# Optimization experiments

Measured on AMD Instinct MI355X. Metric: run time of the kernel, lower is better.

Reference implementation:

```python
import jax, jax.numpy as jnp
import numpy as np

N = 4096
BATCH = 8192


def setup_inputs() -> dict:
    key = jax.random.key(0)
    x = jax.random.normal(key, (BATCH, N), dtype=jnp.float32)
    return {"x": x}


def reference(x):
    # Radix-2 butterfly network (Fast Walsh-Hadamard Transform):
    # at stage s, positions i and i ^ (2**s) are combined as (a+b, a-b).
    B, n = x.shape
    num_stages = int(np.log2(n))
    r = x
    for stage in range(num_stages):  # fixed small loop over log2(n) stages
        stride = 2 ** stage
        # pairs (i, i+stride) live in blocks of 2*stride
        r4 = r.reshape(B, n // (2 * stride), 2, stride)
        a = r4[:, :, 0, :]
        b = r4[:, :, 1, :]
        r = jnp.stack([a + b, a - b], axis=2).reshape(B, n)
    return r
```

## Files before the change

kernel.cpp:

```cpp
#include <hip/hip_runtime.h>


#define N 4096
#define LDS_STRIDE 17

__device__ __forceinline__ void h16(float r[16]) {
    #pragma unroll
    for (int s = 1; s < 16; s <<= 1) {
        #pragma unroll
        for (int m = 0; m < 16; ++m) {
            if (!(m & s)) {
                float x = r[m], y = r[m ^ s];
                r[m]     = x + y;
                r[m ^ s] = x - y;
            }
        }
    }
}

__global__ __launch_bounds__(256) void fwht4096_kernel(const float* __restrict__ in,
                                                       float* __restrict__ out) {
    __shared__ float lds[256 * LDS_STRIDE];

    const int t = threadIdx.x;
    const long long row = blockIdx.x;
    const float* __restrict__ rowIn  = in  + row * (long long)N;
    float* __restrict__       rowOut = out + row * (long long)N;

    float r[16];

    #pragma unroll
    for (int q = 0; q < 4; ++q) {
        const float4 v = *reinterpret_cast<const float4*>(rowIn + t * 16 + q * 4);
        r[q * 4 + 0] = v.x; r[q * 4 + 1] = v.y;
        r[q * 4 + 2] = v.z; r[q * 4 + 3] = v.w;
    }

    h16(r);

    #pragma unroll
    for (int i = 0; i < 16; ++i) lds[LDS_STRIDE * t + i] = r[i];
    __syncthreads();

    const int a = t & 15;
    const int c = t >> 4;
    #pragma unroll
    for (int k = 0; k < 16; ++k)
        r[k] = lds[LDS_STRIDE * (c * 16 + k) + a];

    h16(r);

    __syncthreads();
    #pragma unroll
    for (int k = 0; k < 16; ++k)
        lds[LDS_STRIDE * (c * 16 + k) + a] = r[k];
    __syncthreads();

    const int b = t >> 4;
    #pragma unroll
    for (int k = 0; k < 16; ++k)
        r[k] = lds[LDS_STRIDE * (k * 16 + b) + a];

    h16(r);

    __syncthreads();
    #pragma unroll
    for (int k = 0; k < 16; ++k)
        lds[LDS_STRIDE * (k * 16 + b) + a] = r[k];
    __syncthreads();

    #pragma unroll
    for (int i = 0; i < 16; ++i)
        r[i] = lds[LDS_STRIDE * t + i];

    #pragma unroll
    for (int q = 0; q < 4; ++q) {
        float4 v;
        v.x = r[q * 4 + 0]; v.y = r[q * 4 + 1];
        v.z = r[q * 4 + 2]; v.w = r[q * 4 + 3];
        *reinterpret_cast<float4*>(rowOut + t * 16 + q * 4) = v;
    }
}

extern "C" void kernel_launch(void* const* d_in, const int* in_sizes, int n_in,
                              void* d_out, int out_size, void* d_ws, size_t ws_size,
                              hipStream_t stream) {
    const float* x = (const float*)d_in[0];
    float* y = (float*)d_out;
    const int rows = in_sizes[0] / N;
    fwht4096_kernel<<<rows, 256, 0, stream>>>(x, y);
}
```

Measured before the change: 234.8 us.

## Swizzle LDS layout, drop padding, write final stage directly to global

Replaces the padded LDS (stride 17) with an unpadded 4096-float buffer that uses an XOR swizzle, so the first write can use float4 stores without bank conflicts. The second stage reads and writes back in place with no barrier in between, and the third stage writes straight to global memory with coalesced per-thread strided stores. This removes one LDS round trip and two barriers and reduces LDS usage, and it raises the launch-bounds occupancy hint. The trade-off is scalar global stores in place of float4 stores, plus swizzle index arithmetic.

```diff
diff --git a/kernel.cpp b/kernel.cpp
--- a/kernel.cpp
+++ b/kernel.cpp
@@ -2,7 +2,6 @@
 
 
 #define N 4096
-#define LDS_STRIDE 17
 
 __device__ __forceinline__ void h16(float r[16]) {
     #pragma unroll
@@ -18,9 +17,9 @@
     }
 }
 
-__global__ __launch_bounds__(256) void fwht4096_kernel(const float* __restrict__ in,
-                                                       float* __restrict__ out) {
-    __shared__ float lds[256 * LDS_STRIDE];
+__global__ __launch_bounds__(256, 8) void fwht4096_kernel(const float* __restrict__ in,
+                                                          float* __restrict__ out) {
+    __shared__ float lds[N];
 
     const int t = threadIdx.x;
     const long long row = blockIdx.x;
@@ -30,55 +29,50 @@
     float r[16];
 
     #pragma unroll
-    for (int q = 0; q < 4; ++q) {
-        const float4 v = *reinterpret_cast<const float4*>(rowIn + t * 16 + q * 4);
-        r[q * 4 + 0] = v.x; r[q * 4 + 1] = v.y;
-        r[q * 4 + 2] = v.z; r[q * 4 + 3] = v.w;
+    for (int j = 0; j < 4; ++j) {
+        const float4 v = *reinterpret_cast<const float4*>(rowIn + t * 16 + j * 4);
+        r[j * 4 + 0] = v.x; r[j * 4 + 1] = v.y;
+        r[j * 4 + 2] = v.z; r[j * 4 + 3] = v.w;
     }
 
     h16(r);
 
+    const int x = (t >> 4) & 1;
+    const int s = (t >> 1) & 3;
+    float* wbase = &lds[16 * (t ^ x)];
     #pragma unroll
-    for (int i = 0; i < 16; ++i) lds[LDS_STRIDE * t + i] = r[i];
+    for (int c = 0; c < 4; ++c) {
+        const int i0 = 4 * (c ^ s);
+        const float4 v = make_float4(r[i0], r[i0 + 1], r[i0 + 2], r[i0 + 3]);
+        *reinterpret_cast<float4*>(wbase + 4 * c) = v;
+    }
     __syncthreads();
 
-    const int a = t & 15;
-    const int c = t >> 4;
-    #pragma unroll
-    for (int k = 0; k < 16; ++k)
-        r[k] = lds[LDS_STRIDE * (c * 16 + k) + a];
-
-    h16(r);
-
-    __syncthreads();
-    #pragma unroll
-    for (int k = 0; k < 16; ++k)
-        lds[LDS_STRIDE * (c * 16 + k) + a] = r[k];
+    {
+        const int chi = t >> 4, a = t & 15;
+        const int base = 256 * chi + a;
+        const int fx = (chi & 1) << 4;
+        #pragma unroll
+        for (int k = 0; k < 16; ++k)
+            r[k] = lds[(base + 16 * k) ^ fx ^ (((k >> 1) & 3) << 2)];
+        h16(r);
+        #pragma unroll
+        for (int k = 0; k < 16; ++k)
+            lds[(base + 16 * k) ^ fx ^ (((k >> 1) & 3) << 2)] = r[k];
+    }
     __syncthreads();
 
-    const int b = t >> 4;
-    #pragma unroll
-    for (int k = 0; k < 16; ++k)
-        r[k] = lds[LDS_STRIDE * (k * 16 + b) + a];
-
-    h16(r);
-
-    __syncthreads();
-    #pragma unroll
-    for (int k = 0; k < 16; ++k)
-        lds[LDS_STRIDE * (k * 16 + b) + a] = r[k];
-    __syncthreads();
-
-    #pragma unroll
-    for (int i = 0; i < 16; ++i)
-        r[i] = lds[LDS_STRIDE * t + i];
-
-    #pragma unroll
-    for (int q = 0; q < 4; ++q) {
-        float4 v;
-        v.x = r[q * 4 + 0]; v.y = r[q * 4 + 1];
-        v.z = r[q * 4 + 2]; v.w = r[q * 4 + 3];
-        *reinterpret_cast<float4*>(rowOut + t * 16 + q * 4) = v;
+    {
+        const int b = t >> 4, a = t & 15;
+        const int base = 16 * b + a;
+        const int fb = ((b >> 1) & 3) << 2;
+        #pragma unroll
+        for (int k = 0; k < 16; ++k)
+            r[k] = lds[(256 * k + base) ^ ((k & 1) << 4) ^ fb];
+        h16(r);
+        #pragma unroll
+        for (int k = 0; k < 16; ++k)
+            rowOut[k * 256 + t] = r[k];
     }
 }
 
```

After: 228.2 us. 1.03x faster.
